# Kernel tuning notes

Hardware: AMD Instinct MI355X
Metric: run time of the kernel (lower is better)

The kernel has to match this reference:

```python
import jax, jax.numpy as jnp
import numpy as np

B, L, C = 8, 4096, 1024
M = 16384  # memory bank size


def setup_inputs() -> dict:
    key = jax.random.key(0)
    k_f, k_w1, k_w2, k_mb = jax.random.split(key, 4)
    features = jax.random.normal(k_f, (B, L, C), dtype=jnp.float32)
    # Linear weights stored as (in, out); math identical to torch's x @ W.T + b.
    W1 = jax.random.normal(k_w1, (C, C // 2), dtype=jnp.float32) / np.sqrt(C)
    b1 = jnp.zeros((C // 2,), dtype=jnp.float32)
    W2 = jax.random.normal(k_w2, (C // 2, C // 4), dtype=jnp.float32) / np.sqrt(C // 2)
    b2 = jnp.zeros((C // 4,), dtype=jnp.float32)
    memory_bank = jax.random.normal(k_mb, (M, C // 4), dtype=jnp.float32)
    return {"features": features, "W1": W1, "b1": b1, "W2": W2, "b2": b2,
            "memory_bank": memory_bank}


def reference(features, W1, b1, W2, b2, memory_bank):
    # projection MLP: Linear -> ReLU -> Linear
    h = jax.nn.relu(jnp.einsum('blc,cd->bld', features, W1) + b1)
    proj = jnp.einsum('bld,de->ble', h, W2) + b2          # [B, L, D], D = C//4
    # Euclidean cdist against memory bank, then min over bank entries.
    x2 = jnp.sum(proj * proj, axis=-1, keepdims=True)      # [B, L, 1]
    m2 = jnp.sum(memory_bank * memory_bank, axis=-1)       # [M]
    xm = jnp.einsum('ble,me->blm', proj, memory_bank)      # [B, L, M]
    d2 = jnp.maximum(x2 - 2.0 * xm + m2, 0.0)
    dist = jnp.sqrt(d2)                                    # torch.cdist, p=2
    return jnp.min(dist, axis=-1)                          # [B, L]
```

## Files before the change

### kernel.cpp

```cpp
#include <hip/hip_runtime.h>
#include <math.h>

typedef __bf16 bf16;
typedef __attribute__((ext_vector_type(8))) __bf16 bf16x8;
typedef __attribute__((ext_vector_type(4))) float f32x4;
typedef __attribute__((ext_vector_type(8))) int i32x8;

typedef __attribute__((address_space(1))) const void gvoid;
typedef __attribute__((address_space(3))) void lvoid;
#define GLL(g, l) __builtin_amdgcn_global_load_lds((gvoid*)(g), (lvoid*)(l), 16, 0, 0)
#define MFMA(a, b, c) __builtin_amdgcn_mfma_f32_16x16x32_bf16((a), (b), (c), 0, 0, 0)
#define MFMAS(a, b, c) \
  __builtin_amdgcn_mfma_scale_f32_16x16x128_f8f6f4((a), (b), (c), 0, 0, 0, 0x7F, 0, 0x7F)

__device__ __forceinline__ int swz128(int row, int kb) { return kb ^ ((row & 7) << 4); }

__device__ __forceinline__ unsigned char f32_to_e4m3(float x) {
  const unsigned s = (__float_as_uint(x) >> 24) & 0x80;
  float ax = fminf(fabsf(x), 448.f);
  unsigned e;
  if (ax >= 0.015625f) {
    const unsigned u = __float_as_uint(ax);
    const unsigned t = u + 0x7FFFF + ((u >> 20) & 1);
    e = (((t >> 23) - 120) << 3) | ((t >> 20) & 7);
  } else {
    e = (unsigned)__float2int_rn(ax * 512.f);
  }
  return (unsigned char)(s | e);
}
__device__ __forceinline__ float e4m3_to_f32(unsigned char b) {
  const unsigned s = ((unsigned)b & 0x80) << 24;
  const unsigned em = b & 0x7F;
  float v;
  if (em >= 8) v = __uint_as_float((((em >> 3) + 120) << 23) | ((em & 7) << 20));
  else v = (float)em * 0.001953125f;
  return __uint_as_float(__float_as_uint(v) | s);
}

__global__ __launch_bounds__(256) void prep_w(const float* __restrict__ W1,
                                              const float* __restrict__ W2,
                                              bf16* __restrict__ W1t, bf16* __restrict__ W2t) {
  const int t = blockIdx.x * 256 + threadIdx.x;
  if (t < 512 * 1024) {
    const int h = t & 511, k = t >> 9;
    W1t[h * 1024 + k] = (bf16)W1[k * 512 + h];
  } else {
    const int u = t - 512 * 1024;
    const int e = u & 255, k = u >> 8;
    W2t[e * 512 + k] = (bf16)W2[k * 256 + e];
  }
}

__global__ __launch_bounds__(256) void prep_bank(const float* __restrict__ bank,
                                                 unsigned char* __restrict__ SB8,
                                                 float* __restrict__ m2) {
  const int tid = threadIdx.x, lane = tid & 63, wv = tid >> 6;
  const int row = blockIdx.x * 4 + wv;
  const float4 v = *reinterpret_cast<const float4*>(bank + (size_t)row * 256 + lane * 4);
  uchar4 q;
  float ssum = 0.f;
  {
    const float xs[4] = {v.x, v.y, v.z, v.w};
    unsigned char qb[4];
#pragma unroll
    for (int e = 0; e < 4; ++e) {
      qb[e] = f32_to_e4m3(-2.f * xs[e]);
      const float d = e4m3_to_f32(qb[e]);
      ssum += d * d;
    }
    q.x = qb[0]; q.y = qb[1]; q.z = qb[2]; q.w = qb[3];
  }
#pragma unroll
  for (int off = 1; off < 64; off <<= 1) ssum += __shfl_xor(ssum, off);
  const int t = row >> 7, ww = (row >> 4) & 7, lrr = row & 15;
  const int h = lane >> 5, lk = (lane >> 3) & 3, off32 = (lane & 7) * 4;
  const size_t dst = ((((size_t)t * 8 + ww) * 2 + h) * 64 + lk * 16 + lrr) * 32 + off32;
  *reinterpret_cast<uchar4*>(SB8 + dst) = q;
  if (lane == 0) m2[row] = ssum * 0.25f;
}

__global__ __launch_bounds__(512, 2) void mlp1_kernel(const float* __restrict__ F,
                                                      const bf16* __restrict__ W1t,
                                                      const float* __restrict__ b1,
                                                      bf16* __restrict__ H) {
  __shared__ __align__(16) char smem[81920];
  char* sA = smem;
  char* sB = smem + 16384;

  const int tid = threadIdx.x;
  const int w = tid >> 6, lane = tid & 63;
  const int wm = w >> 2, wn = w & 3;
  const int lr = lane & 15, lk = lane >> 4;
  const size_t r0 = (size_t)blockIdx.x * 128;

  f32x4 acc[4][8];
  const f32x4 z = {0.f, 0.f, 0.f, 0.f};
#pragma unroll
  for (int m = 0; m < 4; ++m)
#pragma unroll
    for (int n = 0; n < 8; ++n) acc[m][n] = z;

  for (int kc = 0; kc < 16; ++kc) {
    {
      const int fr = tid >> 2, kg = (tid & 3) << 4;
      const float* fsrc = F + (r0 + fr) * 1024 + kc * 64 + kg;
      const float4 f0 = *reinterpret_cast<const float4*>(fsrc);
      const float4 f1 = *reinterpret_cast<const float4*>(fsrc + 4);
      const float4 f2 = *reinterpret_cast<const float4*>(fsrc + 8);
      const float4 f3 = *reinterpret_cast<const float4*>(fsrc + 12);
      bf16x8 p0, p1;
      p0[0] = (bf16)f0.x; p0[1] = (bf16)f0.y; p0[2] = (bf16)f0.z; p0[3] = (bf16)f0.w;
      p0[4] = (bf16)f1.x; p0[5] = (bf16)f1.y; p0[6] = (bf16)f1.z; p0[7] = (bf16)f1.w;
      p1[0] = (bf16)f2.x; p1[1] = (bf16)f2.y; p1[2] = (bf16)f2.z; p1[3] = (bf16)f2.w;
      p1[4] = (bf16)f3.x; p1[5] = (bf16)f3.y; p1[6] = (bf16)f3.z; p1[7] = (bf16)f3.w;
      const int bb = kg * 2;
      *(bf16x8*)(sA + fr * 128 + swz128(fr, bb)) = p0;
      *(bf16x8*)(sA + fr * 128 + swz128(fr, bb + 16)) = p1;
    }
#pragma unroll
    for (int i = 0; i < 8; ++i) {
      const int o = (w * 8 + i) * 1024 + lane * 16;
      const int n = o >> 7, b = o & 127;
      GLL((const char*)W1t + n * 2048 + kc * 128 + swz128(n, b), sB + (w * 8 + i) * 1024);
    }
    __syncthreads();
#pragma unroll
    for (int ks = 0; ks < 2; ++ks) {
      bf16x8 av[4];
#pragma unroll
      for (int Mt = 0; Mt < 4; ++Mt) {
        const int row = wm * 64 + Mt * 16 + lr;
        av[Mt] = *(const bf16x8*)(sA + row * 128 + swz128(row, ks * 64 + lk * 16));
      }
#pragma unroll
      for (int Nt = 0; Nt < 8; ++Nt) {
        const int n = wn * 128 + Nt * 16 + lr;
        const bf16x8 bv = *(const bf16x8*)(sB + n * 128 + swz128(n, ks * 64 + lk * 16));
#pragma unroll
        for (int Mt = 0; Mt < 4; ++Mt) acc[Mt][Nt] = MFMA(av[Mt], bv, acc[Mt][Nt]);
      }
    }
    __syncthreads();
  }
#pragma unroll
  for (int Nt = 0; Nt < 8; ++Nt) {
    const int col = wn * 128 + Nt * 16 + lr;
    const float bias = b1[col];
#pragma unroll
    for (int Mt = 0; Mt < 4; ++Mt) {
      const size_t rowb = r0 + wm * 64 + Mt * 16 + lk * 4;
#pragma unroll
      for (int q = 0; q < 4; ++q)
        H[(rowb + q) * 512 + col] = (bf16)fmaxf(acc[Mt][Nt][q] + bias, 0.f);
    }
  }
}

__global__ __launch_bounds__(512, 2) void mlp2_kernel(const bf16* __restrict__ H,
                                                      const bf16* __restrict__ W2t,
                                                      const float* __restrict__ b2,
                                                      unsigned char* __restrict__ PROJ8,
                                                      float* __restrict__ X2) {
  __shared__ __align__(16) char smem[51200];
  char* sA = smem;
  char* sB = smem + 16384;
  float* sX2 = (float*)(smem + 49152);

  const int tid = threadIdx.x;
  const int w = tid >> 6, lane = tid & 63;
  const int wm = w >> 2, wn = w & 3;
  const int lr = lane & 15, lk = lane >> 4;
  const size_t r0 = (size_t)blockIdx.x * 128;

  f32x4 acc[4][4];
  const f32x4 z = {0.f, 0.f, 0.f, 0.f};
#pragma unroll
  for (int m = 0; m < 4; ++m)
#pragma unroll
    for (int n = 0; n < 4; ++n) acc[m][n] = z;

  for (int kc = 0; kc < 8; ++kc) {
#pragma unroll
    for (int i = 0; i < 2; ++i) {
      const int o = (w * 2 + i) * 1024 + lane * 16;
      const int row = o >> 7, b = o & 127;
      GLL((const char*)H + (r0 + row) * 1024 + kc * 128 + swz128(row, b), sA + (w * 2 + i) * 1024);
    }
#pragma unroll
    for (int i = 0; i < 4; ++i) {
      const int o = (w * 4 + i) * 1024 + lane * 16;
      const int n = o >> 7, b = o & 127;
      GLL((const char*)W2t + n * 1024 + kc * 128 + swz128(n, b), sB + (w * 4 + i) * 1024);
    }
    __syncthreads();
#pragma unroll
    for (int ks = 0; ks < 2; ++ks) {
      bf16x8 av[4];
#pragma unroll
      for (int Mt = 0; Mt < 4; ++Mt) {
        const int row = wm * 64 + Mt * 16 + lr;
        av[Mt] = *(const bf16x8*)(sA + row * 128 + swz128(row, ks * 64 + lk * 16));
      }
#pragma unroll
      for (int Nt = 0; Nt < 4; ++Nt) {
        const int n = wn * 64 + Nt * 16 + lr;
        const bf16x8 bv = *(const bf16x8*)(sB + n * 128 + swz128(n, ks * 64 + lk * 16));
#pragma unroll
        for (int Mt = 0; Mt < 4; ++Mt) acc[Mt][Nt] = MFMA(av[Mt], bv, acc[Mt][Nt]);
      }
    }
    __syncthreads();
  }
  float x2p[4][4];
#pragma unroll
  for (int m = 0; m < 4; ++m)
#pragma unroll
    for (int q = 0; q < 4; ++q) x2p[m][q] = 0.f;
#pragma unroll
  for (int Nt = 0; Nt < 4; ++Nt) {
    const int col = wn * 64 + Nt * 16 + lr;
    const float bias = b2[col];
#pragma unroll
    for (int Mt = 0; Mt < 4; ++Mt) {
      const size_t rowb = r0 + wm * 64 + Mt * 16 + lk * 4;
#pragma unroll
      for (int q = 0; q < 4; ++q) {
        const float p = acc[Mt][Nt][q] + bias;
        const unsigned char qb = f32_to_e4m3(p);
        PROJ8[(rowb + q) * 256 + col] = qb;
        const float d = e4m3_to_f32(qb);
        x2p[Mt][q] += d * d;
      }
    }
  }
#pragma unroll
  for (int Mt = 0; Mt < 4; ++Mt)
#pragma unroll
    for (int q = 0; q < 4; ++q) {
      float v = x2p[Mt][q];
      v += __shfl_xor(v, 1); v += __shfl_xor(v, 2);
      v += __shfl_xor(v, 4); v += __shfl_xor(v, 8);
      x2p[Mt][q] = v;
    }
  __syncthreads();
  if (lr == 0) {
#pragma unroll
    for (int Mt = 0; Mt < 4; ++Mt)
#pragma unroll
      for (int q = 0; q < 4; ++q)
        sX2[wn * 128 + wm * 64 + Mt * 16 + lk * 4 + q] = x2p[Mt][q];
  }
  __syncthreads();
  if (tid < 128)
    X2[r0 + tid] = sX2[tid] + sX2[128 + tid] + sX2[256 + tid] + sX2[384 + tid];
}

__global__ __launch_bounds__(512, 2) void dist_kernel(const unsigned char* __restrict__ PROJ8,
                                                      const unsigned char* __restrict__ SB8,
                                                      const float* __restrict__ m2g,
                                                      const float* __restrict__ X2,
                                                      float* __restrict__ out) {
  __shared__ float minbuf[1024];

  const int tid = threadIdx.x;
  const int w = tid >> 6, lane = tid & 63;
  const int lr = lane & 15, lk = lane >> 4;
  const size_t r0 = (size_t)blockIdx.x * 128;

  i32x8 A[8][2];
#pragma unroll
  for (int Mt = 0; Mt < 8; ++Mt)
#pragma unroll
    for (int h = 0; h < 2; ++h)
      A[Mt][h] = *(const i32x8*)(PROJ8 + (r0 + Mt * 16 + lr) * 256 + h * 128 + lk * 32);

  const char* sb = (const char*)SB8 + ((size_t)w * 2 * 64 + lane) * 32;
  const float* m2p = m2g + w * 16 + lr;

  f32x4 minv[8];
#pragma unroll
  for (int Mt = 0; Mt < 8; ++Mt)
#pragma unroll
    for (int q = 0; q < 4; ++q) minv[Mt][q] = 3.0e38f;

#define COMPUTE(B0, B1, MC)                                                       \
  do {                                                                            \
    f32x4 acc[8];                                                                 \
    _Pragma("unroll") for (int Mt = 0; Mt < 8; ++Mt) {                            \
      acc[Mt][0] = (MC); acc[Mt][1] = (MC); acc[Mt][2] = (MC); acc[Mt][3] = (MC); \
    }                                                                             \
    __builtin_amdgcn_s_setprio(1);                                                \
    _Pragma("unroll") for (int Mt = 0; Mt < 8; ++Mt)                              \
      acc[Mt] = MFMAS(A[Mt][0], (B0), acc[Mt]);                                   \
    _Pragma("unroll") for (int Mt = 0; Mt < 8; ++Mt)                              \
      acc[Mt] = MFMAS(A[Mt][1], (B1), acc[Mt]);                                   \
    __builtin_amdgcn_s_setprio(0);                                                \
    _Pragma("unroll") for (int Mt = 0; Mt < 8; ++Mt) {                            \
      minv[Mt][0] = fminf(minv[Mt][0], acc[Mt][0]);                               \
      minv[Mt][1] = fminf(minv[Mt][1], acc[Mt][1]);                               \
      minv[Mt][2] = fminf(minv[Mt][2], acc[Mt][2]);                               \
      minv[Mt][3] = fminf(minv[Mt][3], acc[Mt][3]);                               \
    }                                                                             \
  } while (0)

  i32x8 bA0 = *(const i32x8*)(sb);
  i32x8 bA1 = *(const i32x8*)(sb + 2048);
  float mA = m2p[0];
  i32x8 bB0, bB1;
  float mB;

  for (int t = 0; t < 128; t += 2) {
    bB0 = *(const i32x8*)(sb + (size_t)(t + 1) * 32768);
    bB1 = *(const i32x8*)(sb + (size_t)(t + 1) * 32768 + 2048);
    mB = m2p[(t + 1) * 128];
    __builtin_amdgcn_sched_barrier(0);
    COMPUTE(bA0, bA1, mA);
    bA0 = *(const i32x8*)(sb + (size_t)(t + 2) * 32768);
    bA1 = *(const i32x8*)(sb + (size_t)(t + 2) * 32768 + 2048);
    mA = m2p[(t + 2) * 128];
    __builtin_amdgcn_sched_barrier(0);
    COMPUTE(bB0, bB1, mB);
  }
#undef COMPUTE

#pragma unroll
  for (int Mt = 0; Mt < 8; ++Mt)
#pragma unroll
    for (int q = 0; q < 4; ++q) {
      float v = minv[Mt][q];
      v = fminf(v, __shfl_xor(v, 1)); v = fminf(v, __shfl_xor(v, 2));
      v = fminf(v, __shfl_xor(v, 4)); v = fminf(v, __shfl_xor(v, 8));
      minv[Mt][q] = v;
    }
  if (lr == 0) {
#pragma unroll
    for (int Mt = 0; Mt < 8; ++Mt)
#pragma unroll
      for (int q = 0; q < 4; ++q)
        minbuf[w * 128 + Mt * 16 + lk * 4 + q] = minv[Mt][q];
  }
  __syncthreads();
  if (tid < 128) {
    float m = minbuf[tid];
#pragma unroll
    for (int v = 1; v < 8; ++v) m = fminf(m, minbuf[v * 128 + tid]);
    const float d2 = X2[r0 + tid] + m;
    out[r0 + tid] = sqrtf(fmaxf(d2, 0.f));
  }
}

extern "C" void kernel_launch(void* const* d_in, const int* in_sizes, int n_in,
                              void* d_out, int out_size, void* d_ws, size_t ws_size,
                              hipStream_t stream) {
  const float* F = (const float*)d_in[0];
  const float* W1 = (const float*)d_in[1];
  const float* b1 = (const float*)d_in[2];
  const float* W2 = (const float*)d_in[3];
  const float* b2 = (const float*)d_in[4];
  const float* bank = (const float*)d_in[5];
  float* out = (float*)d_out;

  char* ws = (char*)d_ws;
  unsigned char* SB8 = (unsigned char*)(ws + 0);
  float* m2 = (float*)(ws + 4259840);
  bf16* W1t = (bf16*)(ws + 4326400);
  bf16* W2t = (bf16*)(ws + 5374976);
  bf16* H = (bf16*)(ws + 5637120);
  unsigned char* PROJ8 = (unsigned char*)(ws + 39191552);
  float* X2 = (float*)(ws + 47580160);

  prep_w<<<2560, 256, 0, stream>>>(W1, W2, W1t, W2t);
  prep_bank<<<4096, 256, 0, stream>>>(bank, SB8, m2);
  mlp1_kernel<<<256, 512, 0, stream>>>(F, W1t, b1, H);
  mlp2_kernel<<<256, 512, 0, stream>>>(H, W2t, b2, PROJ8, X2);
  dist_kernel<<<256, 512, 0, stream>>>(PROJ8, SB8, m2, X2, out);
}
```

Before: 209.3 us.

## Halve dist kernel row tile and double grid for higher occupancy

The distance kernel now handles 64 rows per block instead of 128, doubling the grid to 512 blocks and raising launch bounds to allow 4 blocks per CU. The explicit double-buffered bank prefetch with sched barriers is replaced by a simple loop. Smaller register tiles are meant to raise occupancy and fill more CUs, but each bank tile loaded from memory is now reused across half as many rows, doubling bank traffic, and software prefetching is lost.

```diff
diff --git a/kernel.cpp b/kernel.cpp
--- a/kernel.cpp
+++ b/kernel.cpp
@@ -255,21 +255,21 @@
     X2[r0 + tid] = sX2[tid] + sX2[128 + tid] + sX2[256 + tid] + sX2[384 + tid];
 }
 
-__global__ __launch_bounds__(512, 2) void dist_kernel(const unsigned char* __restrict__ PROJ8,
+__global__ __launch_bounds__(512, 4) void dist_kernel(const unsigned char* __restrict__ PROJ8,
                                                       const unsigned char* __restrict__ SB8,
                                                       const float* __restrict__ m2g,
                                                       const float* __restrict__ X2,
                                                       float* __restrict__ out) {
-  __shared__ float minbuf[1024];
+  __shared__ float minbuf[512];
 
   const int tid = threadIdx.x;
   const int w = tid >> 6, lane = tid & 63;
   const int lr = lane & 15, lk = lane >> 4;
-  const size_t r0 = (size_t)blockIdx.x * 128;
-
-  i32x8 A[8][2];
-#pragma unroll
-  for (int Mt = 0; Mt < 8; ++Mt)
+  const size_t r0 = (size_t)blockIdx.x * 64;
+
+  i32x8 A[4][2];
+#pragma unroll
+  for (int Mt = 0; Mt < 4; ++Mt)
 #pragma unroll
     for (int h = 0; h < 2; ++h)
       A[Mt][h] = *(const i32x8*)(PROJ8 + (r0 + Mt * 16 + lr) * 256 + h * 128 + lk * 32);
@@ -277,54 +277,39 @@
   const char* sb = (const char*)SB8 + ((size_t)w * 2 * 64 + lane) * 32;
   const float* m2p = m2g + w * 16 + lr;
 
-  f32x4 minv[8];
-#pragma unroll
-  for (int Mt = 0; Mt < 8; ++Mt)
+  f32x4 minv[4];
+#pragma unroll
+  for (int Mt = 0; Mt < 4; ++Mt)
 #pragma unroll
     for (int q = 0; q < 4; ++q) minv[Mt][q] = 3.0e38f;
 
-#define COMPUTE(B0, B1, MC)                                                       \
-  do {                                                                            \
-    f32x4 acc[8];                                                                 \
-    _Pragma("unroll") for (int Mt = 0; Mt < 8; ++Mt) {                            \
-      acc[Mt][0] = (MC); acc[Mt][1] = (MC); acc[Mt][2] = (MC); acc[Mt][3] = (MC); \
-    }                                                                             \
-    __builtin_amdgcn_s_setprio(1);                                                \
-    _Pragma("unroll") for (int Mt = 0; Mt < 8; ++Mt)                              \
-      acc[Mt] = MFMAS(A[Mt][0], (B0), acc[Mt]);                                   \
-    _Pragma("unroll") for (int Mt = 0; Mt < 8; ++Mt)                              \
-      acc[Mt] = MFMAS(A[Mt][1], (B1), acc[Mt]);                                   \
-    __builtin_amdgcn_s_setprio(0);                                                \
-    _Pragma("unroll") for (int Mt = 0; Mt < 8; ++Mt) {                            \
-      minv[Mt][0] = fminf(minv[Mt][0], acc[Mt][0]);                               \
-      minv[Mt][1] = fminf(minv[Mt][1], acc[Mt][1]);                               \
-      minv[Mt][2] = fminf(minv[Mt][2], acc[Mt][2]);                               \
-      minv[Mt][3] = fminf(minv[Mt][3], acc[Mt][3]);                               \
-    }                                                                             \
-  } while (0)
-
-  i32x8 bA0 = *(const i32x8*)(sb);
-  i32x8 bA1 = *(const i32x8*)(sb + 2048);
-  float mA = m2p[0];
-  i32x8 bB0, bB1;
-  float mB;
-
-  for (int t = 0; t < 128; t += 2) {
-    bB0 = *(const i32x8*)(sb + (size_t)(t + 1) * 32768);
-    bB1 = *(const i32x8*)(sb + (size_t)(t + 1) * 32768 + 2048);
-    mB = m2p[(t + 1) * 128];
-    __builtin_amdgcn_sched_barrier(0);
-    COMPUTE(bA0, bA1, mA);
-    bA0 = *(const i32x8*)(sb + (size_t)(t + 2) * 32768);
-    bA1 = *(const i32x8*)(sb + (size_t)(t + 2) * 32768 + 2048);
-    mA = m2p[(t + 2) * 128];
-    __builtin_amdgcn_sched_barrier(0);
-    COMPUTE(bB0, bB1, mB);
-  }
-#undef COMPUTE
-
-#pragma unroll
-  for (int Mt = 0; Mt < 8; ++Mt)
+  for (int t = 0; t < 128; ++t) {
+    const i32x8 B0 = *(const i32x8*)(sb + (size_t)t * 32768);
+    const i32x8 B1 = *(const i32x8*)(sb + (size_t)t * 32768 + 2048);
+    const float m2c = m2p[t * 128];
+
+    f32x4 acc[4];
+#pragma unroll
+    for (int Mt = 0; Mt < 4; ++Mt) {
+      acc[Mt][0] = m2c; acc[Mt][1] = m2c; acc[Mt][2] = m2c; acc[Mt][3] = m2c;
+    }
+    __builtin_amdgcn_s_setprio(1);
+#pragma unroll
+    for (int Mt = 0; Mt < 4; ++Mt) acc[Mt] = MFMAS(A[Mt][0], B0, acc[Mt]);
+#pragma unroll
+    for (int Mt = 0; Mt < 4; ++Mt) acc[Mt] = MFMAS(A[Mt][1], B1, acc[Mt]);
+    __builtin_amdgcn_s_setprio(0);
+#pragma unroll
+    for (int Mt = 0; Mt < 4; ++Mt) {
+      minv[Mt][0] = fminf(minv[Mt][0], acc[Mt][0]);
+      minv[Mt][1] = fminf(minv[Mt][1], acc[Mt][1]);
+      minv[Mt][2] = fminf(minv[Mt][2], acc[Mt][2]);
+      minv[Mt][3] = fminf(minv[Mt][3], acc[Mt][3]);
+    }
+  }
+
+#pragma unroll
+  for (int Mt = 0; Mt < 4; ++Mt)
 #pragma unroll
     for (int q = 0; q < 4; ++q) {
       float v = minv[Mt][q];
@@ -334,16 +319,16 @@
     }
   if (lr == 0) {
 #pragma unroll
-    for (int Mt = 0; Mt < 8; ++Mt)
+    for (int Mt = 0; Mt < 4; ++Mt)
 #pragma unroll
       for (int q = 0; q < 4; ++q)
-        minbuf[w * 128 + Mt * 16 + lk * 4 + q] = minv[Mt][q];
+        minbuf[w * 64 + Mt * 16 + lk * 4 + q] = minv[Mt][q];
   }
   __syncthreads();
-  if (tid < 128) {
+  if (tid < 64) {
     float m = minbuf[tid];
 #pragma unroll
-    for (int v = 1; v < 8; ++v) m = fminf(m, minbuf[v * 128 + tid]);
+    for (int v = 1; v < 8; ++v) m = fminf(m, minbuf[v * 64 + tid]);
     const float d2 = X2[r0 + tid] + m;
     out[r0 + tid] = sqrtf(fmaxf(d2, 0.f));
   }
@@ -373,5 +358,5 @@
   prep_bank<<<4096, 256, 0, stream>>>(bank, SB8, m2);
   mlp1_kernel<<<256, 512, 0, stream>>>(F, W1t, b1, H);
   mlp2_kernel<<<256, 512, 0, stream>>>(H, W2t, b2, PROJ8, X2);
-  dist_kernel<<<256, 512, 0, stream>>>(PROJ8, SB8, m2, X2, out);
-}
+  dist_kernel<<<512, 512, 0, stream>>>(PROJ8, SB8, m2, X2, out);
+}
```

Measured after the change: 316.7 us. +51.3%, slower.
